# Performance work log

Measured on AMD Instinct MI355X. Metric: run time of the kernel, lower is better.

Reference implementation:

```python
import jax, jax.numpy as jnp
import numpy as np

N, E = 100000, 1600000
IN_C, HID, NUM_CLASSES = 128, 256, 15
EPS = 1e-5


def setup_inputs() -> dict:
    key = jax.random.key(0)
    ks = jax.random.split(key, 20)

    def lin(k, out_c, in_c):
        # torch Linear default init: U(-1/sqrt(in), 1/sqrt(in))
        bound = 1.0 / np.sqrt(in_c)
        return jax.random.uniform(k, (out_c, in_c), jnp.float32, -bound, bound)

    inp = {
        'x': jax.random.normal(ks[0], (N, IN_C), jnp.float32),
        'edge_index': jax.random.randint(ks[1], (2, E), 0, N, jnp.int64),
        # conv1: SAGEConv(IN_C -> HID): lin_l (with bias) on aggregated msgs, lin_r (no bias) on root
        'w1_l': lin(ks[2], HID, IN_C), 'b1_l': jnp.zeros((HID,), jnp.float32), 'w1_r': lin(ks[3], HID, IN_C),
        'g1': jnp.ones((HID,), jnp.float32), 'be1': jnp.zeros((HID,), jnp.float32),
        # conv2: HID -> HID
        'w2_l': lin(ks[4], HID, HID), 'b2_l': jnp.zeros((HID,), jnp.float32), 'w2_r': lin(ks[5], HID, HID),
        'g2': jnp.ones((HID,), jnp.float32), 'be2': jnp.zeros((HID,), jnp.float32),
        # conv3: HID -> HID//2
        'w3_l': lin(ks[6], HID // 2, HID), 'b3_l': jnp.zeros((HID // 2,), jnp.float32), 'w3_r': lin(ks[7], HID // 2, HID),
        'g3': jnp.ones((HID // 2,), jnp.float32), 'be3': jnp.zeros((HID // 2,), jnp.float32),
        # classifier
        'wc': lin(ks[8], NUM_CLASSES, HID // 2), 'bc': jnp.zeros((NUM_CLASSES,), jnp.float32),
    }
    return inp


def _sage(x, src, dst, w_l, b_l, w_r):
    # PyG SAGEConv (aggr='mean'): lin_l(mean_{j in N(i)} x_j) + lin_r(x_i)
    n = x.shape[0]
    agg = jax.ops.segment_sum(x[src], dst, num_segments=n)            # [N, d]
    deg = jax.ops.segment_sum(jnp.ones_like(dst, dtype=x.dtype), dst, num_segments=n)
    mean = agg / jnp.maximum(deg, 1.0)[:, None]
    return mean @ w_l.T + b_l + x @ w_r.T


def _bn_relu(x, g, b):
    # BatchNorm1d in training mode: biased batch stats over node dim, then ReLU
    mu = jnp.mean(x, axis=0)
    var = jnp.mean((x - mu) ** 2, axis=0)
    return jax.nn.relu((x - mu) * jax.lax.rsqrt(var + EPS) * g + b)


def reference(x, edge_index, w1_l, b1_l, w1_r, g1, be1, w2_l, b2_l, w2_r, g2, be2,
              w3_l, b3_l, w3_r, g3, be3, wc, bc):
    src, dst = edge_index[0], edge_index[1]
    h = _bn_relu(_sage(x, src, dst, w1_l, b1_l, w1_r), g1, be1)   # dropout = identity (eval)
    h = _bn_relu(_sage(h, src, dst, w2_l, b2_l, w2_r), g2, be2)
    h = _bn_relu(_sage(h, src, dst, w3_l, b3_l, w3_r), g3, be3)
    return h @ wc.T + bc
```

## Files before the change

### kernel.cpp

```cpp
#include <hip/hip_runtime.h>


#define DEV static __device__ __forceinline__

typedef unsigned short us;
typedef __attribute__((ext_vector_type(8))) __bf16 bf16x8;
typedef __attribute__((ext_vector_type(4))) float f32x4;

DEV float bf2f(us u) { return __uint_as_float(((unsigned)u) << 16); }
DEV us f2bf(float f) {
    unsigned u = __float_as_uint(f);
    unsigned r = u + 0x7fffu + ((u >> 16) & 1u);
    return (us)(r >> 16);
}

typedef __attribute__((address_space(3))) void lds_void;
typedef const __attribute__((address_space(1))) void gbl_void;
DEV void gll16(const void* g, void* l) {
    __builtin_amdgcn_global_load_lds((gbl_void*)g, (lds_void*)l, 16, 0, 0);
}

DEV bool is_i64(const int* ei) {
    return (ei[1] == 0) & (ei[3] == 0) & (ei[5] == 0) & (ei[7] == 0);
}


__global__ void bucket_hist(const int* __restrict__ ei, int E, int* __restrict__ hist2,
                            int NB, int chunk) {
    __shared__ int h[256];
    const int g = blockIdx.x, t = threadIdx.x;
    const bool i64 = is_i64(ei);
    h[t] = 0;
    __syncthreads();
    int beg = g * chunk, end = min(beg + chunk, E);
    for (int e = beg + t; e < end; e += 256) {
        int d = i64 ? ei[2 * (E + e)] : ei[E + e];
        atomicAdd(&h[d >> 9], 1);
    }
    __syncthreads();
    if (t < NB) hist2[g * NB + t] = h[t];
}

__global__ void bucket_offsets(int* __restrict__ hist2, int* __restrict__ bucketBase,
                               int* __restrict__ rp, int N, int G, int NB) {
    __shared__ int tot[256];
    const int t = threadIdx.x;
    int sum = 0;
    if (t < NB)
        for (int g = 0; g < G; ++g) sum += hist2[g * NB + t];
    tot[t] = sum;
    __syncthreads();
    for (int off = 1; off < 256; off <<= 1) {
        int v = (t >= off) ? tot[t - off] : 0;
        __syncthreads();
        tot[t] += v;
        __syncthreads();
    }
    int base = tot[t] - sum;
    if (t < NB) {
        bucketBase[t] = base;
        int run = base;
        for (int g = 0; g < G; ++g) {
            int v = hist2[g * NB + t];
            hist2[g * NB + t] = run;
            run += v;
        }
        if (t == NB - 1) {
            bucketBase[NB] = tot[t];
            rp[N] = tot[t];
        }
    }
}

__global__ void scatter8(const int* __restrict__ ei, int E, const int* __restrict__ hist2,
                         uint2* __restrict__ ebuf, int NB, int chunk) {
    __shared__ int off[256];
    const int g = blockIdx.x, t = threadIdx.x;
    const bool i64 = is_i64(ei);
    if (t < NB) off[t] = hist2[g * NB + t];
    __syncthreads();
    int beg = g * chunk, end = min(beg + chunk, E);
    for (int e = beg + t; e < end; e += 256) {
        int s = i64 ? ei[2 * e] : ei[e];
        int d = i64 ? ei[2 * (E + e)] : ei[E + e];
        int p = atomicAdd(&off[d >> 9], 1);
        ebuf[p] = make_uint2((unsigned)s, (unsigned)d);
    }
}

__global__ void fine_csr(const uint2* __restrict__ ebuf, const int* __restrict__ bucketBase,
                         int N, int* __restrict__ rp, int* __restrict__ csr) {
    __shared__ int cnt[512];
    __shared__ int red[256];
    const int b = blockIdx.x, t = threadIdx.x;
    const int node0 = b << 9;
    cnt[t] = 0;
    cnt[t + 256] = 0;
    __syncthreads();
    const int ebeg = bucketBase[b], eend = bucketBase[b + 1];
    for (int e = ebeg + t; e < eend; e += 256) {
        uint2 r = ebuf[e];
        atomicAdd(&cnt[r.y & 511], 1);
    }
    __syncthreads();
    int c0 = cnt[2 * t], c1 = cnt[2 * t + 1];
    int s = c0 + c1;
    red[t] = s;
    __syncthreads();
    for (int off = 1; off < 256; off <<= 1) {
        int v = (t >= off) ? red[t - off] : 0;
        __syncthreads();
        red[t] += v;
        __syncthreads();
    }
    int pre = red[t] - s;
    int n0 = node0 + 2 * t;
    if (n0 < N) rp[n0] = ebeg + pre;
    if (n0 + 1 < N) rp[n0 + 1] = ebeg + pre + c0;
    __syncthreads();
    cnt[2 * t] = ebeg + pre;
    cnt[2 * t + 1] = ebeg + pre + c0;
    __syncthreads();
    for (int e = ebeg + t; e < eend; e += 256) {
        uint2 r = ebuf[e];
        int p = atomicAdd(&cnt[r.y & 511], 1);
        csr[p] = (int)r.x;
    }
}


struct WSeg { const float* s; us* d; int n4; int l2w4; int stride; };
struct WConvAll { WSeg seg[8]; };

__global__ void conv_all(WConvAll wc) {
    for (int sg = 0; sg < 8; ++sg) {
        WSeg w = wc.seg[sg];
        for (int i = blockIdx.x * blockDim.x + threadIdx.x; i < w.n4; i += gridDim.x * blockDim.x) {
            float4 v = ((const float4*)w.s)[i];
            ushort4 r;
            r.x = f2bf(v.x); r.y = f2bf(v.y); r.z = f2bf(v.z); r.w = f2bf(v.w);
            int row = i >> w.l2w4;
            int col = (i - (row << w.l2w4)) * 4;
            *(ushort4*)(w.d + (size_t)row * w.stride + col) = r;
        }
    }
}


template <int VEC>
__global__ void agg_mean(const us* __restrict__ X, const int* __restrict__ rp,
                         const int* __restrict__ csr, us* __restrict__ M, int n) {
    const int cols = VEC * 64;
    int w = blockIdx.x * (blockDim.x >> 6) + (threadIdx.x >> 6);
    int lane = threadIdx.x & 63;
    if (w >= n) return;
    int beg = rp[w], end = rp[w + 1];
    const us* Xb = X + lane * VEC;
    float acc[VEC];
#pragma unroll
    for (int i = 0; i < VEC; ++i) acc[i] = 0.f;
    int e = beg;
    for (; e + 4 <= end; e += 4) {
        int j0 = csr[e], j1 = csr[e + 1], j2 = csr[e + 2], j3 = csr[e + 3];
        if (VEC == 2) {
            unsigned u0 = *(const unsigned*)(Xb + (size_t)j0 * cols);
            unsigned u1 = *(const unsigned*)(Xb + (size_t)j1 * cols);
            unsigned u2 = *(const unsigned*)(Xb + (size_t)j2 * cols);
            unsigned u3 = *(const unsigned*)(Xb + (size_t)j3 * cols);
            acc[0] += __uint_as_float(u0 << 16) + __uint_as_float(u1 << 16)
                    + __uint_as_float(u2 << 16) + __uint_as_float(u3 << 16);
            acc[1] += __uint_as_float(u0 & 0xffff0000u) + __uint_as_float(u1 & 0xffff0000u)
                    + __uint_as_float(u2 & 0xffff0000u) + __uint_as_float(u3 & 0xffff0000u);
        } else {
            uint2 u0 = *(const uint2*)(Xb + (size_t)j0 * cols);
            uint2 u1 = *(const uint2*)(Xb + (size_t)j1 * cols);
            uint2 u2 = *(const uint2*)(Xb + (size_t)j2 * cols);
            uint2 u3 = *(const uint2*)(Xb + (size_t)j3 * cols);
            acc[0] += __uint_as_float(u0.x << 16) + __uint_as_float(u1.x << 16)
                    + __uint_as_float(u2.x << 16) + __uint_as_float(u3.x << 16);
            acc[1] += __uint_as_float(u0.x & 0xffff0000u) + __uint_as_float(u1.x & 0xffff0000u)
                    + __uint_as_float(u2.x & 0xffff0000u) + __uint_as_float(u3.x & 0xffff0000u);
            acc[2] += __uint_as_float(u0.y << 16) + __uint_as_float(u1.y << 16)
                    + __uint_as_float(u2.y << 16) + __uint_as_float(u3.y << 16);
            acc[3] += __uint_as_float(u0.y & 0xffff0000u) + __uint_as_float(u1.y & 0xffff0000u)
                    + __uint_as_float(u2.y & 0xffff0000u) + __uint_as_float(u3.y & 0xffff0000u);
        }
    }
    for (; e < end; ++e) {
        int j0 = csr[e];
        if (VEC == 2) {
            unsigned u0 = *(const unsigned*)(Xb + (size_t)j0 * cols);
            acc[0] += __uint_as_float(u0 << 16);
            acc[1] += __uint_as_float(u0 & 0xffff0000u);
        } else {
            uint2 u0 = *(const uint2*)(Xb + (size_t)j0 * cols);
            acc[0] += __uint_as_float(u0.x << 16);
            acc[1] += __uint_as_float(u0.x & 0xffff0000u);
            acc[2] += __uint_as_float(u0.y << 16);
            acc[3] += __uint_as_float(u0.y & 0xffff0000u);
        }
    }
    float inv = 1.0f / (float)max(end - beg, 1);
    us* q = M + (size_t)w * cols + lane * VEC;
    if (VEC == 2) {
        *(ushort2*)q = make_ushort2(f2bf(acc[0] * inv), f2bf(acc[1] * inv));
    } else {
        *(ushort4*)q = make_ushort4(f2bf(acc[0] * inv), f2bf(acc[1] * inv),
                                    f2bf(acc[2] * inv), f2bf(acc[3] * inv));
    }
}

__global__ void agg_post(const us* __restrict__ Yc, const int* __restrict__ rp,
                         const int* __restrict__ csr, const float* __restrict__ bias,
                         us* __restrict__ H, int n) {
    int w = blockIdx.x * (blockDim.x >> 6) + (threadIdx.x >> 6);
    int lane = threadIdx.x & 63;
    if (w >= n) return;
    int beg = rp[w], end = rp[w + 1];
    const us* Yb = Yc + lane * 2;
    float a0 = 0.f, a1 = 0.f;
    int e = beg;
    for (; e + 4 <= end; e += 4) {
        int j0 = csr[e], j1 = csr[e + 1], j2 = csr[e + 2], j3 = csr[e + 3];
        unsigned u0 = *(const unsigned*)(Yb + (size_t)j0 * 256);
        unsigned u1 = *(const unsigned*)(Yb + (size_t)j1 * 256);
        unsigned u2 = *(const unsigned*)(Yb + (size_t)j2 * 256);
        unsigned u3 = *(const unsigned*)(Yb + (size_t)j3 * 256);
        a0 += __uint_as_float(u0 << 16) + __uint_as_float(u1 << 16)
            + __uint_as_float(u2 << 16) + __uint_as_float(u3 << 16);
        a1 += __uint_as_float(u0 & 0xffff0000u) + __uint_as_float(u1 & 0xffff0000u)
            + __uint_as_float(u2 & 0xffff0000u) + __uint_as_float(u3 & 0xffff0000u);
    }
    for (; e < end; ++e) {
        unsigned u0 = *(const unsigned*)(Yb + (size_t)csr[e] * 256);
        a0 += __uint_as_float(u0 << 16);
        a1 += __uint_as_float(u0 & 0xffff0000u);
    }
    float inv = 1.0f / (float)max(end - beg, 1);
    unsigned uz = *(const unsigned*)(Yc + (size_t)w * 256 + 128 + lane * 2);
    float2 bv = *(const float2*)(bias + lane * 2);
    float r0 = a0 * inv + __uint_as_float(uz << 16) + bv.x;
    float r1 = a1 * inv + __uint_as_float(uz & 0xffff0000u) + bv.y;
    *(ushort2*)(H + (size_t)w * 128 + lane * 2) = make_ushort2(f2bf(r0), f2bf(r1));
}


template <int THREADS, int BM, int BN, int WM, int WN>
__launch_bounds__(THREADS)
__global__ void gemm_mfma(const us* __restrict__ A0, int K0,
                          const us* __restrict__ A1, int K1,
                          const us* __restrict__ W, const float* __restrict__ bias,
                          int n, int outc, us* __restrict__ Cbf, float* __restrict__ Cf,
                          float* __restrict__ st0, float* __restrict__ st1) {
    constexpr int MT = WM / 16;
    constexpr int NT = WN / 16;
    constexpr int WCols = BN / WN;
    constexpr int NDMA = (BM * 4 + BN * 4) / THREADS;
    static_assert((BM * 4) % THREADS == 0 && (BN * 4) % THREADS == 0, "uniform DMA");
    static_assert((BM / WM) * (BN / WN) == THREADS / 64, "wave tiling");
    __shared__ __align__(16) us As[2][BM * 32];
    __shared__ __align__(16) us Bs[2][BN * 32];
    __shared__ float colred[2][BN];

    const int t = threadIdx.x;
    const int wid = t >> 6, lane = t & 63;
    const int wr = wid / WCols, wcc = wid % WCols;
    const int row0 = blockIdx.x * BM;
    const int col0 = blockIdx.y * BN;
    const int Kp = K0 + K1;
    const int nk = Kp >> 5;
    const int l15 = lane & 15, l4 = lane >> 4;

    auto issue = [&](int kidx, int p) {
        int kc = kidx << 5;
        const us* A = (kc < K0) ? A0 : A1;
        int rs = (kc < K0) ? K0 : K1;
        int ko = (kc < K0) ? kc : kc - K0;
#pragma unroll
        for (int c = t; c < BM * 4; c += THREADS) {
            int blk = c >> 6;
            int row = row0 + (blk << 4) + l15;
            gll16(A + (size_t)row * rs + ko + (l4 << 3), (char*)As[p] + blk * 1024 + lane * 16);
        }
#pragma unroll
        for (int c = t; c < BN * 4; c += THREADS) {
            int blk = c >> 6;
            int col = col0 + (blk << 4) + l15;
            gll16(W + (size_t)col * Kp + kc + (l4 << 3), (char*)Bs[p] + blk * 1024 + lane * 16);
        }
    };

    f32x4 acc[MT][NT];
#pragma unroll
    for (int i = 0; i < MT; ++i)
#pragma unroll
        for (int j = 0; j < NT; ++j) acc[i][j] = (f32x4){0.f, 0.f, 0.f, 0.f};

    issue(0, 0);
    if (nk > 1) issue(1, 1);
    for (int k = 0; k < nk; ++k) {
        if (k + 1 < nk) asm volatile("s_waitcnt vmcnt(%0)" :: "i"(NDMA) : "memory");
        else            asm volatile("s_waitcnt vmcnt(0)" ::: "memory");
        asm volatile("s_barrier" ::: "memory");
        const int p = k & 1;
        bf16x8 af[MT], bfr[NT];
#pragma unroll
        for (int mt = 0; mt < MT; ++mt)
            af[mt] = *(const bf16x8*)((char*)As[p] + (wr * MT + mt) * 1024 + lane * 16);
#pragma unroll
        for (int nt = 0; nt < NT; ++nt)
            bfr[nt] = *(const bf16x8*)((char*)Bs[p] + (wcc * NT + nt) * 1024 + lane * 16);
#pragma unroll
        for (int mt = 0; mt < MT; ++mt)
#pragma unroll
            for (int nt = 0; nt < NT; ++nt)
                acc[mt][nt] = __builtin_amdgcn_mfma_f32_16x16x32_bf16(af[mt], bfr[nt], acc[mt][nt], 0, 0, 0);
        if (k + 2 < nk) {
            asm volatile("s_barrier" ::: "memory");
            issue(k + 2, p);
        }
    }

    if (st0) {
#pragma unroll
        for (int c = t; c < 2 * BN; c += THREADS) (&colred[0][0])[c] = 0.f;
        __syncthreads();
    }

#pragma unroll
    for (int nt = 0; nt < NT; ++nt) {
        int col = col0 + wcc * WN + nt * 16 + l15;
        bool cok = col < outc;
        float bv = (bias != nullptr && cok) ? bias[col] : 0.f;
        float ls = 0.f, lq = 0.f;
#pragma unroll
        for (int mt = 0; mt < MT; ++mt) {
            int rbase = row0 + wr * WM + mt * 16 + (l4 << 2);
#pragma unroll
            for (int i = 0; i < 4; ++i) {
                int r = rbase + i;
                if (r < n && cok) {
                    float v = acc[mt][nt][i] + bv;
                    if (Cf) Cf[(size_t)r * outc + col] = v;
                    else Cbf[(size_t)r * outc + col] = f2bf(v);
                    ls += v;
                    lq += v * v;
                }
            }
        }
        if (st0 && cok) {
            int lc = wcc * WN + nt * 16 + l15;
            atomicAdd(&colred[0][lc], ls);
            atomicAdd(&colred[1][lc], lq);
        }
    }
    if (st0) {
        __syncthreads();
        int rep = (blockIdx.x & 7) << 8;
        for (int c = t; c < BN; c += THREADS) {
            if (col0 + c < outc) {
                atomicAdd(&st0[rep + col0 + c], colred[0][c]);
                atomicAdd(&st1[rep + col0 + c], colred[1][c]);
            }
        }
    }
}


__global__ void bn_stats(const us* __restrict__ H, int n, int c,
                         float* __restrict__ s0, float* __restrict__ s1) {
    int col = threadIdx.x;
    if (col >= c) return;
    float s = 0.f, q = 0.f;
    for (int r = blockIdx.x; r < n; r += gridDim.x) {
        float v = bf2f(H[(size_t)r * c + col]);
        s += v;
        q += v * v;
    }
    int rep = (blockIdx.x & 7) << 8;
    atomicAdd(&s0[rep + col], s);
    atomicAdd(&s1[rep + col], q);
}

__global__ void bn_apply(us* __restrict__ H, int n8, int c,
                         const float* __restrict__ s0, const float* __restrict__ s1,
                         const float* __restrict__ g, const float* __restrict__ be, float fn) {
    __shared__ float sc[256], sh[256];
    int t = threadIdx.x;
    if (t < c) {
        float s = 0.f, q = 0.f;
#pragma unroll
        for (int r = 0; r < 8; ++r) {
            s += s0[(r << 8) + t];
            q += s1[(r << 8) + t];
        }
        float mean = s / fn;
        float var = q / fn - mean * mean;
        float scale = g[t] * rsqrtf(var + 1e-5f);
        sc[t] = scale;
        sh[t] = be[t] - mean * scale;
    }
    __syncthreads();
    int cdiv8 = c >> 3;
    for (int i = blockIdx.x * blockDim.x + t; i < n8; i += gridDim.x * blockDim.x) {
        int col = (i % cdiv8) << 3;
        uint4 v = ((const uint4*)H)[i];
        float f[8];
        f[0] = __uint_as_float(v.x << 16); f[1] = __uint_as_float(v.x & 0xffff0000u);
        f[2] = __uint_as_float(v.y << 16); f[3] = __uint_as_float(v.y & 0xffff0000u);
        f[4] = __uint_as_float(v.z << 16); f[5] = __uint_as_float(v.z & 0xffff0000u);
        f[6] = __uint_as_float(v.w << 16); f[7] = __uint_as_float(v.w & 0xffff0000u);
        float4 sc0 = *(const float4*)&sc[col];
        float4 sc1 = *(const float4*)&sc[col + 4];
        float4 sh0 = *(const float4*)&sh[col];
        float4 sh1 = *(const float4*)&sh[col + 4];
        f[0] = fmaxf(f[0] * sc0.x + sh0.x, 0.f);
        f[1] = fmaxf(f[1] * sc0.y + sh0.y, 0.f);
        f[2] = fmaxf(f[2] * sc0.z + sh0.z, 0.f);
        f[3] = fmaxf(f[3] * sc0.w + sh0.w, 0.f);
        f[4] = fmaxf(f[4] * sc1.x + sh1.x, 0.f);
        f[5] = fmaxf(f[5] * sc1.y + sh1.y, 0.f);
        f[6] = fmaxf(f[6] * sc1.z + sh1.z, 0.f);
        f[7] = fmaxf(f[7] * sc1.w + sh1.w, 0.f);
        uint4 o;
        o.x = (unsigned)f2bf(f[0]) | ((unsigned)f2bf(f[1]) << 16);
        o.y = (unsigned)f2bf(f[2]) | ((unsigned)f2bf(f[3]) << 16);
        o.z = (unsigned)f2bf(f[4]) | ((unsigned)f2bf(f[5]) << 16);
        o.w = (unsigned)f2bf(f[6]) | ((unsigned)f2bf(f[7]) << 16);
        ((uint4*)H)[i] = o;
    }
}


extern "C" void kernel_launch(void* const* d_in, const int* in_sizes, int n_in,
                              void* d_out, int out_size, void* d_ws, size_t ws_size,
                              hipStream_t stream) {
    const float* x = (const float*)d_in[0];
    const int* ei = (const int*)d_in[1];
    const float* w1_l = (const float*)d_in[2];
    const float* b1_l = (const float*)d_in[3];
    const float* w1_r = (const float*)d_in[4];
    const float* g1 = (const float*)d_in[5];
    const float* be1 = (const float*)d_in[6];
    const float* w2_l = (const float*)d_in[7];
    const float* b2_l = (const float*)d_in[8];
    const float* w2_r = (const float*)d_in[9];
    const float* g2 = (const float*)d_in[10];
    const float* be2 = (const float*)d_in[11];
    const float* w3_l = (const float*)d_in[12];
    const float* b3_l = (const float*)d_in[13];
    const float* w3_r = (const float*)d_in[14];
    const float* g3 = (const float*)d_in[15];
    const float* be3 = (const float*)d_in[16];
    const float* wcf = (const float*)d_in[17];
    const float* bc = (const float*)d_in[18];

    const int N = in_sizes[0] / 128;
    const int E = in_sizes[1] / 2;
    const int NB = (N + 511) >> 9;
    const int G = 256;
    const int chunk = (E + G - 1) / G;

    char* ws = (char*)d_ws;
    size_t off = 0;
    auto alloc = [&](size_t bytes) -> char* {
        char* p = ws + off;
        off += (bytes + 255) & ~(size_t)255;
        return p;
    };
    int* rp = (int*)alloc((size_t)(N + 1) * 4);
    int* csr = (int*)alloc((size_t)E * 4);
    int* hist2 = (int*)alloc((size_t)G * NB * 4);
    int* bucketBase = (int*)alloc((size_t)(NB + 1) * 4);
    uint2* ebuf = (uint2*)alloc((size_t)E * 8);
    us* xbf = (us*)alloc((size_t)N * 128 * 2);
    us* M = (us*)alloc((size_t)N * 256 * 2);
    us* Ha = (us*)alloc((size_t)N * 256 * 2);
    us* Hb = (us*)alloc((size_t)N * 256 * 2);
    float* stats = (float*)alloc(6 * 8 * 256 * 4);
    float* s01 = stats,          *s11 = stats + 2048;
    float* s02 = stats + 4096,   *s12 = stats + 6144;
    float* s03 = stats + 8192,   *s13 = stats + 10240;
    us* wcat1 = (us*)alloc(256 * 256 * 2);
    us* wcat2 = (us*)alloc(256 * 512 * 2);
    us* w3cat = (us*)alloc(256 * 256 * 2);
    us* wc_b = (us*)alloc(64 * 128 * 2);
    alloc(1 << 20);
    (void)ws_size; (void)n_in; (void)out_size;

    hipMemsetAsync(stats, 0, 6 * 8 * 256 * 4, stream);
    WConvAll wc;
    wc.seg[0] = {x,    xbf,         N * 128 / 4,  5, 128};
    wc.seg[1] = {w1_l, wcat1,       256 * 128 / 4, 5, 256};
    wc.seg[2] = {w1_r, wcat1 + 128, 256 * 128 / 4, 5, 256};
    wc.seg[3] = {w2_l, wcat2,       256 * 256 / 4, 6, 512};
    wc.seg[4] = {w2_r, wcat2 + 256, 256 * 256 / 4, 6, 512};
    wc.seg[5] = {w3_l, w3cat,             128 * 256 / 4, 6, 256};
    wc.seg[6] = {w3_r, w3cat + 128 * 256, 128 * 256 / 4, 6, 256};
    wc.seg[7] = {wcf,  wc_b,        15 * 128 / 4,  5, 128};
    conv_all<<<1024, 256, 0, stream>>>(wc);
    bucket_hist<<<G, 256, 0, stream>>>(ei, E, hist2, NB, chunk);
    bucket_offsets<<<1, 256, 0, stream>>>(hist2, bucketBase, rp, N, G, NB);
    scatter8<<<G, 256, 0, stream>>>(ei, E, hist2, ebuf, NB, chunk);
    fine_csr<<<NB, 256, 0, stream>>>(ebuf, bucketBase, N, rp, csr);

    const int aggGrid = (N + 3) / 4;
    const int rowTiles = (N + 127) / 128;

    agg_mean<2><<<aggGrid, 256, 0, stream>>>(xbf, rp, csr, M, N);
    gemm_mfma<512, 128, 256, 64, 64><<<rowTiles, 512, 0, stream>>>(
        M, 128, xbf, 128, wcat1, b1_l, N, 256, Ha, nullptr, s01, s11);
    bn_apply<<<2048, 256, 0, stream>>>(Ha, N * 256 / 8, 256, s01, s11, g1, be1, (float)N);

    agg_mean<4><<<aggGrid, 256, 0, stream>>>(Ha, rp, csr, M, N);
    gemm_mfma<512, 128, 256, 64, 64><<<rowTiles, 512, 0, stream>>>(
        M, 256, Ha, 256, wcat2, b2_l, N, 256, Hb, nullptr, s02, s12);
    bn_apply<<<2048, 256, 0, stream>>>(Hb, N * 256 / 8, 256, s02, s12, g2, be2, (float)N);

    gemm_mfma<512, 128, 256, 64, 64><<<rowTiles, 512, 0, stream>>>(
        Hb, 256, nullptr, 0, w3cat, nullptr, N, 256, M, nullptr, nullptr, nullptr);
    agg_post<<<aggGrid, 256, 0, stream>>>(M, rp, csr, b3_l, Ha, N);
    bn_stats<<<1024, 256, 0, stream>>>(Ha, N, 128, s03, s13);
    bn_apply<<<2048, 256, 0, stream>>>(Ha, N * 128 / 8, 128, s03, s13, g3, be3, (float)N);

    gemm_mfma<256, 128, 64, 128, 16><<<rowTiles, 256, 0, stream>>>(
        Ha, 128, nullptr, 0, wc_b, bc, N, 15, nullptr, (float*)d_out, nullptr, nullptr);
}
```

Baseline: 798.5 us.

## Fuse final BN+classifier, unroll gathers by 8, parallelize bucket offsets, fold memset

Replaces the last bn_apply plus tiny MFMA classifier GEMM with one fused kernel that applies BN3+ReLU on the fly and computes the 15 logits per row in FP32 from LDS weights. This removes a full read/write pass over the 128-wide activation. The mean-aggregation and agg_post gathers are unrolled to 8 independent loads to raise memory-level parallelism. bucket_offsets now uses 1024 threads so each thread sums a quarter of the groups, and the stats memset is folded into conv_all. The fused classifier uses scalar per-thread row loads and 15 accumulators, which may be less efficient than the MFMA path.

```diff
diff --git a/kernel.cpp b/kernel.cpp
--- a/kernel.cpp
+++ b/kernel.cpp
@@ -1,4 +1,5 @@
 #include <hip/hip_runtime.h>
+#include <type_traits>
 
 
 #define DEV static __device__ __forceinline__
@@ -12,6 +13,10 @@
     unsigned u = __float_as_uint(f);
     unsigned r = u + 0x7fffu + ((u >> 16) & 1u);
     return (us)(r >> 16);
+}
+DEV void acc2(float* a, unsigned u) {
+    a[0] += __uint_as_float(u << 16);
+    a[1] += __uint_as_float(u & 0xffff0000u);
 }
 
 typedef __attribute__((address_space(3))) void lds_void;
@@ -43,31 +48,41 @@
 
 __global__ void bucket_offsets(int* __restrict__ hist2, int* __restrict__ bucketBase,
                                int* __restrict__ rp, int N, int G, int NB) {
+    __shared__ int part[1024];
     __shared__ int tot[256];
     const int t = threadIdx.x;
+    const int b = t & 255, q = t >> 8;
     int sum = 0;
-    if (t < NB)
-        for (int g = 0; g < G; ++g) sum += hist2[g * NB + t];
-    tot[t] = sum;
+    if (b < NB)
+        for (int g = q * 64; g < q * 64 + 64; ++g) sum += hist2[g * NB + b];
+    part[q * 256 + b] = sum;
+    __syncthreads();
+    if (t < 256)
+        tot[t] = part[t] + part[256 + t] + part[512 + t] + part[768 + t];
     __syncthreads();
     for (int off = 1; off < 256; off <<= 1) {
-        int v = (t >= off) ? tot[t - off] : 0;
+        int v = 0;
+        if (t < 256 && t >= off) v = tot[t - off];
         __syncthreads();
-        tot[t] += v;
+        if (t < 256) tot[t] += v;
         __syncthreads();
     }
-    int base = tot[t] - sum;
-    if (t < NB) {
-        bucketBase[t] = base;
+    if (b < NB) {
+        int sumb = part[b] + part[256 + b] + part[512 + b] + part[768 + b];
+        int base = tot[b] - sumb;
+        if (q == 0) {
+            bucketBase[b] = base;
+            if (b == NB - 1) {
+                bucketBase[NB] = tot[b];
+                rp[N] = tot[b];
+            }
+        }
         int run = base;
-        for (int g = 0; g < G; ++g) {
-            int v = hist2[g * NB + t];
-            hist2[g * NB + t] = run;
+        for (int qq = 0; qq < q; ++qq) run += part[qq * 256 + b];
+        for (int g = q * 64; g < q * 64 + 64; ++g) {
+            int v = hist2[g * NB + b];
+            hist2[g * NB + b] = run;
             run += v;
-        }
-        if (t == NB - 1) {
-            bucketBase[NB] = tot[t];
-            rp[N] = tot[t];
         }
     }
 }
@@ -132,7 +147,10 @@
 struct WSeg { const float* s; us* d; int n4; int l2w4; int stride; };
 struct WConvAll { WSeg seg[8]; };
 
-__global__ void conv_all(WConvAll wc) {
+__global__ void conv_all(WConvAll wc, float* __restrict__ stats, int nstats) {
+    if (blockIdx.x == 0) {
+        for (int i = threadIdx.x; i < nstats; i += blockDim.x) stats[i] = 0.f;
+    }
     for (int sg = 0; sg < 8; ++sg) {
         WSeg w = wc.seg[sg];
         for (int i = blockIdx.x * blockDim.x + threadIdx.x; i < w.n4; i += gridDim.x * blockDim.x) {
@@ -156,48 +174,48 @@
     if (w >= n) return;
     int beg = rp[w], end = rp[w + 1];
     const us* Xb = X + lane * VEC;
-    float acc[VEC];
-#pragma unroll
-    for (int i = 0; i < VEC; ++i) acc[i] = 0.f;
+    using LT = typename std::conditional<VEC == 2, unsigned, uint2>::type;
+    float acc[VEC] = {};
     int e = beg;
-    for (; e + 4 <= end; e += 4) {
-        int j0 = csr[e], j1 = csr[e + 1], j2 = csr[e + 2], j3 = csr[e + 3];
+    for (; e + 8 <= end; e += 8) {
+        int j[8];
+#pragma unroll
+        for (int u = 0; u < 8; ++u) j[u] = csr[e + u];
+        LT v[8];
+#pragma unroll
+        for (int u = 0; u < 8; ++u) v[u] = *(const LT*)(Xb + (size_t)j[u] * cols);
+#pragma unroll
+        for (int u = 0; u < 8; ++u) {
+            if (VEC == 2) {
+                acc2(acc, *(const unsigned*)&v[u]);
+            } else {
+                const uint2* p = (const uint2*)&v[u];
+                acc2(acc, p->x);
+                acc2(acc + 2, p->y);
+            }
+        }
+    }
+    for (; e + 2 <= end; e += 2) {
+        int j0 = csr[e], j1 = csr[e + 1];
+        LT v0 = *(const LT*)(Xb + (size_t)j0 * cols);
+        LT v1 = *(const LT*)(Xb + (size_t)j1 * cols);
         if (VEC == 2) {
-            unsigned u0 = *(const unsigned*)(Xb + (size_t)j0 * cols);
-            unsigned u1 = *(const unsigned*)(Xb + (size_t)j1 * cols);
-            unsigned u2 = *(const unsigned*)(Xb + (size_t)j2 * cols);
-            unsigned u3 = *(const unsigned*)(Xb + (size_t)j3 * cols);
-            acc[0] += __uint_as_float(u0 << 16) + __uint_as_float(u1 << 16)
-                    + __uint_as_float(u2 << 16) + __uint_as_float(u3 << 16);
-            acc[1] += __uint_as_float(u0 & 0xffff0000u) + __uint_as_float(u1 & 0xffff0000u)
-                    + __uint_as_float(u2 & 0xffff0000u) + __uint_as_float(u3 & 0xffff0000u);
+            acc2(acc, *(const unsigned*)&v0);
+            acc2(acc, *(const unsigned*)&v1);
         } else {
-            uint2 u0 = *(const uint2*)(Xb + (size_t)j0 * cols);
-            uint2 u1 = *(const uint2*)(Xb + (size_t)j1 * cols);
-            uint2 u2 = *(const uint2*)(Xb + (size_t)j2 * cols);
-            uint2 u3 = *(const uint2*)(Xb + (size_t)j3 * cols);
-            acc[0] += __uint_as_float(u0.x << 16) + __uint_as_float(u1.x << 16)
-                    + __uint_as_float(u2.x << 16) + __uint_as_float(u3.x << 16);
-            acc[1] += __uint_as_float(u0.x & 0xffff0000u) + __uint_as_float(u1.x & 0xffff0000u)
-                    + __uint_as_float(u2.x & 0xffff0000u) + __uint_as_float(u3.x & 0xffff0000u);
-            acc[2] += __uint_as_float(u0.y << 16) + __uint_as_float(u1.y << 16)
-                    + __uint_as_float(u2.y << 16) + __uint_as_float(u3.y << 16);
-            acc[3] += __uint_as_float(u0.y & 0xffff0000u) + __uint_as_float(u1.y & 0xffff0000u)
-                    + __uint_as_float(u2.y & 0xffff0000u) + __uint_as_float(u3.y & 0xffff0000u);
-        }
-    }
-    for (; e < end; ++e) {
-        int j0 = csr[e];
+            const uint2* p0 = (const uint2*)&v0;
+            const uint2* p1 = (const uint2*)&v1;
+            acc2(acc, p0->x); acc2(acc + 2, p0->y);
+            acc2(acc, p1->x); acc2(acc + 2, p1->y);
+        }
+    }
+    if (e < end) {
+        LT v0 = *(const LT*)(Xb + (size_t)csr[e] * cols);
         if (VEC == 2) {
-            unsigned u0 = *(const unsigned*)(Xb + (size_t)j0 * cols);
-            acc[0] += __uint_as_float(u0 << 16);
-            acc[1] += __uint_as_float(u0 & 0xffff0000u);
+            acc2(acc, *(const unsigned*)&v0);
         } else {
-            uint2 u0 = *(const uint2*)(Xb + (size_t)j0 * cols);
-            acc[0] += __uint_as_float(u0.x << 16);
-            acc[1] += __uint_as_float(u0.x & 0xffff0000u);
-            acc[2] += __uint_as_float(u0.y << 16);
-            acc[3] += __uint_as_float(u0.y & 0xffff0000u);
+            const uint2* p0 = (const uint2*)&v0;
+            acc2(acc, p0->x); acc2(acc + 2, p0->y);
         }
     }
     float inv = 1.0f / (float)max(end - beg, 1);
@@ -218,29 +236,30 @@
     if (w >= n) return;
     int beg = rp[w], end = rp[w + 1];
     const us* Yb = Yc + lane * 2;
-    float a0 = 0.f, a1 = 0.f;
+    float a[2] = {};
     int e = beg;
-    for (; e + 4 <= end; e += 4) {
-        int j0 = csr[e], j1 = csr[e + 1], j2 = csr[e + 2], j3 = csr[e + 3];
-        unsigned u0 = *(const unsigned*)(Yb + (size_t)j0 * 256);
-        unsigned u1 = *(const unsigned*)(Yb + (size_t)j1 * 256);
-        unsigned u2 = *(const unsigned*)(Yb + (size_t)j2 * 256);
-        unsigned u3 = *(const unsigned*)(Yb + (size_t)j3 * 256);
-        a0 += __uint_as_float(u0 << 16) + __uint_as_float(u1 << 16)
-            + __uint_as_float(u2 << 16) + __uint_as_float(u3 << 16);
-        a1 += __uint_as_float(u0 & 0xffff0000u) + __uint_as_float(u1 & 0xffff0000u)
-            + __uint_as_float(u2 & 0xffff0000u) + __uint_as_float(u3 & 0xffff0000u);
-    }
-    for (; e < end; ++e) {
-        unsigned u0 = *(const unsigned*)(Yb + (size_t)csr[e] * 256);
-        a0 += __uint_as_float(u0 << 16);
-        a1 += __uint_as_float(u0 & 0xffff0000u);
-    }
+    for (; e + 8 <= end; e += 8) {
+        int j[8];
+#pragma unroll
+        for (int u = 0; u < 8; ++u) j[u] = csr[e + u];
+        unsigned v[8];
+#pragma unroll
+        for (int u = 0; u < 8; ++u) v[u] = *(const unsigned*)(Yb + (size_t)j[u] * 256);
+#pragma unroll
+        for (int u = 0; u < 8; ++u) acc2(a, v[u]);
+    }
+    for (; e + 2 <= end; e += 2) {
+        unsigned v0 = *(const unsigned*)(Yb + (size_t)csr[e] * 256);
+        unsigned v1 = *(const unsigned*)(Yb + (size_t)csr[e + 1] * 256);
+        acc2(a, v0);
+        acc2(a, v1);
+    }
+    if (e < end) acc2(a, *(const unsigned*)(Yb + (size_t)csr[e] * 256));
     float inv = 1.0f / (float)max(end - beg, 1);
     unsigned uz = *(const unsigned*)(Yc + (size_t)w * 256 + 128 + lane * 2);
     float2 bv = *(const float2*)(bias + lane * 2);
-    float r0 = a0 * inv + __uint_as_float(uz << 16) + bv.x;
-    float r1 = a1 * inv + __uint_as_float(uz & 0xffff0000u) + bv.y;
+    float r0 = a[0] * inv + __uint_as_float(uz << 16) + bv.x;
+    float r1 = a[1] * inv + __uint_as_float(uz & 0xffff0000u) + bv.y;
     *(ushort2*)(H + (size_t)w * 128 + lane * 2) = make_ushort2(f2bf(r0), f2bf(r1));
 }
 
@@ -432,6 +451,55 @@
 }
 
 
+__global__ void cls_fused(const us* __restrict__ H, int n,
+                          const float* __restrict__ s0, const float* __restrict__ s1,
+                          const float* __restrict__ g, const float* __restrict__ be, float fn,
+                          const us* __restrict__ wcb, const float* __restrict__ bc,
+                          float* __restrict__ out) {
+    __shared__ float sc[128], sh[128], wl[15][128], bcs[15];
+    int t = threadIdx.x;
+    if (t < 128) {
+        float s = 0.f, q = 0.f;
+#pragma unroll
+        for (int r = 0; r < 8; ++r) {
+            s += s0[(r << 8) + t];
+            q += s1[(r << 8) + t];
+        }
+        float mean = s / fn;
+        float var = q / fn - mean * mean;
+        float scale = g[t] * rsqrtf(var + 1e-5f);
+        sc[t] = scale;
+        sh[t] = be[t] - mean * scale;
+    }
+    for (int i = t; i < 15 * 128; i += blockDim.x) wl[i >> 7][i & 127] = bf2f(wcb[i]);
+    if (t < 15) bcs[t] = bc[t];
+    __syncthreads();
+    for (int r = blockIdx.x * blockDim.x + t; r < n; r += gridDim.x * blockDim.x) {
+        const uint4* hp = (const uint4*)(H + (size_t)r * 128);
+        float acc[15] = {};
+#pragma unroll
+        for (int k8 = 0; k8 < 16; ++k8) {
+            uint4 v = hp[k8];
+            float f[8];
+            f[0] = __uint_as_float(v.x << 16); f[1] = __uint_as_float(v.x & 0xffff0000u);
+            f[2] = __uint_as_float(v.y << 16); f[3] = __uint_as_float(v.y & 0xffff0000u);
+            f[4] = __uint_as_float(v.z << 16); f[5] = __uint_as_float(v.z & 0xffff0000u);
+            f[6] = __uint_as_float(v.w << 16); f[7] = __uint_as_float(v.w & 0xffff0000u);
+            int kb = k8 << 3;
+#pragma unroll
+            for (int j = 0; j < 8; ++j) {
+                float hv = fmaxf(f[j] * sc[kb + j] + sh[kb + j], 0.f);
+#pragma unroll
+                for (int c = 0; c < 15; ++c) acc[c] += hv * wl[c][kb + j];
+            }
+        }
+        float* op = out + (size_t)r * 15;
+#pragma unroll
+        for (int c = 0; c < 15; ++c) op[c] = acc[c] + bcs[c];
+    }
+}
+
+
 extern "C" void kernel_launch(void* const* d_in, const int* in_sizes, int n_in,
                               void* d_out, int out_size, void* d_ws, size_t ws_size,
                               hipStream_t stream) {
@@ -484,11 +552,10 @@
     us* wcat1 = (us*)alloc(256 * 256 * 2);
     us* wcat2 = (us*)alloc(256 * 512 * 2);
     us* w3cat = (us*)alloc(256 * 256 * 2);
-    us* wc_b = (us*)alloc(64 * 128 * 2);
+    us* wc_b = (us*)alloc(16 * 128 * 2);
     alloc(1 << 20);
     (void)ws_size; (void)n_in; (void)out_size;
 
-    hipMemsetAsync(stats, 0, 6 * 8 * 256 * 4, stream);
     WConvAll wc;
     wc.seg[0] = {x,    xbf,         N * 128 / 4,  5, 128};
     wc.seg[1] = {w1_l, wcat1,       256 * 128 / 4, 5, 256};
@@ -498,9 +565,9 @@
     wc.seg[5] = {w3_l, w3cat,             128 * 256 / 4, 6, 256};
     wc.seg[6] = {w3_r, w3cat + 128 * 256, 128 * 256 / 4, 6, 256};
     wc.seg[7] = {wcf,  wc_b,        15 * 128 / 4,  5, 128};
-    conv_all<<<1024, 256, 0, stream>>>(wc);
+    conv_all<<<1024, 256, 0, stream>>>(wc, stats, 6 * 8 * 256);
     bucket_hist<<<G, 256, 0, stream>>>(ei, E, hist2, NB, chunk);
-    bucket_offsets<<<1, 256, 0, stream>>>(hist2, bucketBase, rp, N, G, NB);
+    bucket_offsets<<<1, 1024, 0, stream>>>(hist2, bucketBase, rp, N, G, NB);
     scatter8<<<G, 256, 0, stream>>>(ei, E, hist2, ebuf, NB, chunk);
     fine_csr<<<NB, 256, 0, stream>>>(ebuf, bucketBase, N, rp, csr);
 
@@ -521,8 +588,7 @@
         Hb, 256, nullptr, 0, w3cat, nullptr, N, 256, M, nullptr, nullptr, nullptr);
     agg_post<<<aggGrid, 256, 0, stream>>>(M, rp, csr, b3_l, Ha, N);
     bn_stats<<<1024, 256, 0, stream>>>(Ha, N, 128, s03, s13);
-    bn_apply<<<2048, 256, 0, stream>>>(Ha, N * 128 / 8, 128, s03, s13, g3, be3, (float)N);
-
-    gemm_mfma<256, 128, 64, 128, 16><<<rowTiles, 256, 0, stream>>>(
-        Ha, 128, nullptr, 0, wc_b, bc, N, 15, nullptr, (float*)d_out, nullptr, nullptr);
-}
+
+    cls_fused<<<512, 256, 0, stream>>>(Ha, N, s03, s13, g3, be3, (float)N, wc_b, bc,
+                                       (float*)d_out);
+}
```

Result: no change. 806.9 us (+1.1%).
